# Kernel tuning notes

Hardware: AMD Instinct MI355X
Metric: run time of the kernel (lower is better)

The kernel has to match this reference:

```python
import jax, jax.numpy as jnp
import numpy as np

BQ, BK = 128, 64  # SpargeAttn-style Q/K block sizes
NEG = -1e30


def _block_mask(q, k, simthreshd1, cdfthreshd, scale):
    """Mean-similarity block selection: a (q-block, k-block) pair is pruned only
    when both blocks are self-similar (mean cosine sim to block mean exceeds the
    per-head simthreshd1) AND it is not in the top-CDF mass (cdfthreshd) of the
    compressed block-level softmax."""
    B, H, L, D = q.shape
    nq, nk = L // BQ, L // BK
    qb = q.reshape(B, H, nq, BQ, D)
    kb = k.reshape(B, H, nk, BK, D)
    qm = qb.mean(3)  # [B,H,nq,D] block means
    km = kb.mean(3)  # [B,H,nk,D]

    def blocksim(xb, xm):
        xn = xb / (jnp.linalg.norm(xb, axis=-1, keepdims=True) + 1e-6)
        mn = xm / (jnp.linalg.norm(xm, axis=-1, keepdims=True) + 1e-6)
        return jnp.einsum('bhntd,bhnd->bhnt', xn, mn).mean(-1)  # [B,H,n]

    th = simthreshd1[None, :, None]
    comp_q = blocksim(qb, qm) > th  # [B,H,nq] self-similar q blocks
    comp_k = blocksim(kb, km) > th  # [B,H,nk]

    # compressed attention over block means, then CDF-based top-mass selection
    p = jax.nn.softmax(jnp.einsum('bhqd,bhkd->bhqk', qm, km) * scale, axis=-1)
    order = jnp.argsort(-p, axis=-1)
    sp = jnp.take_along_axis(p, order, axis=-1)
    csum = jnp.cumsum(sp, axis=-1)
    keep_sorted = (csum - sp) < cdfthreshd[None, :, None, None]  # prefix covering tau
    rank = jnp.argsort(order, axis=-1)  # inverse permutation
    selected = jnp.take_along_axis(keep_sorted, rank, axis=-1)  # [B,H,nq,nk]

    return selected | ~(comp_q[..., :, None] & comp_k[..., None, :])


def setup_inputs() -> dict:
    key = jax.random.key(0)
    kq, kk, kv, kc = jax.random.split(key, 4)
    B, H, L, D = 1, 16, 2048, 64
    return {
        'q': jax.random.normal(kq, (B, H, L, D), dtype=jnp.float32),
        'k': jax.random.normal(kk, (B, H, L, D), dtype=jnp.float32),
        'v': jax.random.normal(kv, (B, H, L, D), dtype=jnp.float32),
        'simthreshd1': jnp.zeros((H,), dtype=jnp.float32),
        'cdfthreshd': jax.random.uniform(kc, (H,), dtype=jnp.float32),
    }


def reference(q, k, v, simthreshd1, cdfthreshd):
    B, H, L, D = q.shape
    scale = 1.0 / np.sqrt(D).astype(np.float32)
    # smooth_k: subtract per-(B,H) key mean (softmax-invariant shift, matches kernel)
    k = k - k.mean(axis=-2, keepdims=True)
    bmask = _block_mask(q, k, simthreshd1, cdfthreshd, scale)  # [B,H,nq,nk] bool
    mask_tok = jnp.repeat(jnp.repeat(bmask, BQ, axis=2), BK, axis=3)  # [B,H,L,L]
    s = jnp.einsum('bhqd,bhkd->bhqk', q, k) * scale
    s = jnp.where(mask_tok, s, NEG)
    p = jax.nn.softmax(s, axis=-1)
    return jnp.einsum('bhqk,bhkd->bhqd', p, v)
```

## Files before the change

kernel.cpp:

```cpp
#include <hip/hip_runtime.h>

#define HH 16
#define LL 2048
#define DD 64
#define BQ 128
#define BK 64
#define NQ (LL/BQ)
#define NK (LL/BK)
#define SCALE 0.125f
#define QSCALE (0.125f * 1.44269504f)

typedef __attribute__((ext_vector_type(8))) short s8v;
typedef __attribute__((ext_vector_type(4))) float f4v;

static __device__ __forceinline__ ushort f2bf(float x) {
    unsigned u = __float_as_uint(x);
    u += 0x7fff + ((u >> 16) & 1);
    return (ushort)(u >> 16);
}

#define GLOAD(src, dst) \
    __builtin_amdgcn_global_load_lds((const __attribute__((address_space(1))) unsigned int*)(src), \
                                     (__attribute__((address_space(3))) unsigned int*)(dst), 16, 0, 0)

__global__ void kmean1_kernel(const float* __restrict__ k, float* __restrict__ kpart) {
    int b = blockIdx.x;
    int h = blockIdx.y;
    int t = threadIdx.x;
    int d = t & 63, c = t >> 6;
    const float* kh = k + ((size_t)h*LL + (size_t)b*256) * DD;
    float s = 0.f;
    for (int l = c*64; l < c*64 + 64; ++l) s += kh[(size_t)l * DD + d];
    __shared__ float red[4][64];
    red[c][d] = s;
    __syncthreads();
    if (t < 64) kpart[((size_t)h*8 + b)*64 + t] = red[0][t]+red[1][t]+red[2][t]+red[3][t];
}

__global__ void qstat_kernel(const float* __restrict__ q, const float* __restrict__ simth,
                             float* __restrict__ qm, int* __restrict__ compq,
                             ushort* __restrict__ qb) {
    int qi = blockIdx.x, h = blockIdx.y;
    int t = threadIdx.x;
    size_t row = (size_t)h*LL + (size_t)qi*BQ + t;
    const float* rp = q + row * DD;
    float x[DD]; float n2 = 0.f;
    #pragma unroll
    for (int d = 0; d < DD; d += 4) {
        float4 v4 = *(const float4*)(rp + d);
        x[d]=v4.x; x[d+1]=v4.y; x[d+2]=v4.z; x[d+3]=v4.w;
        n2 += v4.x*v4.x + v4.y*v4.y + v4.z*v4.z + v4.w*v4.w;
    }
    #pragma unroll
    for (int d = 0; d < DD; d += 4) {
        ushort4 o;
        o.x = f2bf(x[d]*QSCALE);   o.y = f2bf(x[d+1]*QSCALE);
        o.z = f2bf(x[d+2]*QSCALE); o.w = f2bf(x[d+3]*QSCALE);
        *(ushort4*)(qb + row*DD + d) = o;
    }
    __shared__ float xs[BQ][DD+1];
    #pragma unroll
    for (int d = 0; d < DD; ++d) xs[t][d] = x[d];
    __syncthreads();
    __shared__ float mean[DD];
    if (t < DD) {
        float s = 0.f;
        for (int r = 0; r < BQ; ++r) s += xs[r][t];
        mean[t] = s * (1.0f/BQ);
    }
    __syncthreads();
    float dot = 0.f, m2 = 0.f;
    #pragma unroll
    for (int d = 0; d < DD; ++d) { dot += x[d]*mean[d]; m2 += mean[d]*mean[d]; }
    float cs = dot / ((sqrtf(n2) + 1e-6f) * (sqrtf(m2) + 1e-6f));
    __shared__ float red[BQ];
    red[t] = cs; __syncthreads();
    for (int sft = BQ/2; sft > 0; sft >>= 1) {
        if (t < sft) red[t] += red[t + sft];
        __syncthreads();
    }
    if (t == 0) compq[h*NQ + qi] = (red[0] * (1.0f/BQ)) > simth[h] ? 1 : 0;
    if (t < DD) qm[((size_t)h*NQ + qi)*DD + t] = mean[t];
}

__global__ void kstat_kernel(const float* __restrict__ k, const float* __restrict__ v,
                             const float* __restrict__ kpart, const float* __restrict__ simth,
                             float* __restrict__ km, int* __restrict__ compk,
                             ushort* __restrict__ kb, ushort* __restrict__ vTb) {
    int ki = blockIdx.x, h = blockIdx.y;
    int t = threadIdx.x;
    __shared__ float mu_s[DD];
    {
        float s = 0.f;
        #pragma unroll
        for (int b = 0; b < 8; ++b) s += kpart[((size_t)h*8 + b)*64 + t];
        mu_s[t] = s * (1.0f/LL);
    }
    __syncthreads();
    size_t row = (size_t)h*LL + (size_t)ki*BK + t;
    const float* rp = k + row * DD;
    float x[DD]; float n2 = 0.f;
    #pragma unroll
    for (int d = 0; d < DD; d += 4) {
        float4 v4 = *(const float4*)(rp + d);
        v4.x -= mu_s[d]; v4.y -= mu_s[d+1]; v4.z -= mu_s[d+2]; v4.w -= mu_s[d+3];
        x[d]=v4.x; x[d+1]=v4.y; x[d+2]=v4.z; x[d+3]=v4.w;
        n2 += v4.x*v4.x + v4.y*v4.y + v4.z*v4.z + v4.w*v4.w;
    }
    #pragma unroll
    for (int d = 0; d < DD; d += 4) {
        ushort4 o;
        o.x = f2bf(x[d]);   o.y = f2bf(x[d+1]);
        o.z = f2bf(x[d+2]); o.w = f2bf(x[d+3]);
        *(ushort4*)(kb + row*DD + d) = o;
    }
    __shared__ ushort vs[64][66];
    {
        const float* vp = v + row * DD;
        #pragma unroll
        for (int d = 0; d < DD; d += 4) {
            float4 v4 = *(const float4*)(vp + d);
            vs[t][d]   = f2bf(v4.x); vs[t][d+1] = f2bf(v4.y);
            vs[t][d+2] = f2bf(v4.z); vs[t][d+3] = f2bf(v4.w);
        }
    }
    __shared__ float xs[BK][DD+1];
    #pragma unroll
    for (int d = 0; d < DD; ++d) xs[t][d] = x[d];
    __syncthreads();
    {
        size_t vbase = ((size_t)h*DD + t)*LL + (size_t)ki*64;
        #pragma unroll
        for (int r8 = 0; r8 < 64; r8 += 8) {
            s8v o;
            #pragma unroll
            for (int e = 0; e < 8; ++e) o[e] = (short)vs[r8+e][t];
            *(s8v*)(vTb + vbase + r8) = o;
        }
    }
    __shared__ float mean[DD];
    {
        float s = 0.f;
        for (int r = 0; r < BK; ++r) s += xs[r][t];
        mean[t] = s * (1.0f/BK);
    }
    __syncthreads();
    float dot = 0.f, m2 = 0.f;
    #pragma unroll
    for (int d = 0; d < DD; ++d) { dot += x[d]*mean[d]; m2 += mean[d]*mean[d]; }
    float cs = dot / ((sqrtf(n2) + 1e-6f) * (sqrtf(m2) + 1e-6f));
    __shared__ float red[BK];
    red[t] = cs; __syncthreads();
    for (int sft = BK/2; sft > 0; sft >>= 1) {
        if (t < sft) red[t] += red[t + sft];
        __syncthreads();
    }
    if (t == 0) compk[h*NK + ki] = (red[0] * (1.0f/BK)) > simth[h] ? 1 : 0;
    km[((size_t)h*NK + ki)*DD + t] = mean[t];
}

__global__ void bmask_kernel(const float* __restrict__ qm, const float* __restrict__ km,
                             const int* __restrict__ compq, const int* __restrict__ compk,
                             const float* __restrict__ cdfth, unsigned* __restrict__ bmaskbits) {
    int qi = blockIdx.x, h = blockIdx.y;
    int j = threadIdx.x;
    __shared__ float ssh[NK];
    __shared__ float p[NK];
    const float* qv = qm + ((size_t)h*NQ + qi)*DD;
    const float* kv = km + ((size_t)h*NK + j)*DD;
    float s = 0.f;
    for (int d = 0; d < DD; ++d) s += qv[d]*kv[d];
    ssh[j] = s * SCALE;
    __syncthreads();
    float m = ssh[0];
    for (int i = 1; i < NK; ++i) m = fmaxf(m, ssh[i]);
    float den = 0.f;
    for (int i = 0; i < NK; ++i) den += expf(ssh[i] - m);
    p[j] = expf(ssh[j] - m) / den;
    __syncthreads();
    float pj = p[j];
    float mass = 0.f;
    for (int i = 0; i < NK; ++i) {
        float pi = p[i];
        if (pi > pj || (pi == pj && i < j)) mass += pi;
    }
    int sel = (mass < cdfth[h]) ? 1 : 0;
    int keep = (sel || !(compq[h*NQ+qi] && compk[h*NK+j])) ? 1 : 0;
    unsigned long long bal = __ballot(keep);
    if (j == 0) bmaskbits[h*NQ + qi] = (unsigned)bal;
}

__global__ __launch_bounds__(256, 2) void attn_kernel(
        const ushort* __restrict__ qb, const ushort* __restrict__ kb,
        const ushort* __restrict__ vTb, const unsigned* __restrict__ bmaskbits,
        float* __restrict__ out) {
    __shared__ __align__(16) ushort ldsK[2][64*64];
    __shared__ __align__(16) ushort ldsV[2][64*64];
    __shared__ __align__(16) ushort plds[4][16][72];

    int h    = blockIdx.y;
    int qi   = blockIdx.x >> 1;
    int half = blockIdx.x & 1;
    int tid  = threadIdx.x;
    int w    = tid >> 6;
    int l    = tid & 63;
    int lo = l & 15, hi = l >> 4;
    int r0 = qi*BQ + half*64 + w*16;

    unsigned msk = bmaskbits[h*NQ + qi];

    const ushort* qh = qb  + (size_t)h*LL*DD;
    const char*   kh = (const char*)(kb  + (size_t)h*LL*DD);
    const char*   vh = (const char*)(vTb + (size_t)h*DD*LL);

    int srow = l >> 3;
    int sgx  = ((l & 7) ^ srow) * 16;
    int c0 = 2*w, c1 = 2*w + 1;
    size_t ks0 = (size_t)(c0*8 + srow)*128 + sgx;
    size_t ks1 = (size_t)(c1*8 + srow)*128 + sgx;
    size_t vs0 = (size_t)(c0*8 + srow)*(LL*2) + sgx;
    size_t vs1 = (size_t)(c1*8 + srow)*(LL*2) + sgx;
    int dst0 = c0*1024, dst1 = c1*1024;

    int p0 = (hi)     ^ (lo & 7);
    int p1 = (4 + hi) ^ (lo & 7);
    int kidx0 = lo*64 + p0*8;
    int kidx1 = lo*64 + p1*8;

    s8v qa[2];
    #pragma unroll
    for (int kk = 0; kk < 2; ++kk)
        qa[kk] = *(const s8v*)(qh + (size_t)(r0 + lo)*DD + kk*32 + hi*8);

    f4v O[4];
    float mrun = -1e30f, lrun = 0.f;
    #pragma unroll
    for (int nd = 0; nd < 4; ++nd) O[nd] = (f4v){0.f, 0.f, 0.f, 0.f};

    auto stage = [&](int buf, int j) {
        const char* kj = kh + (size_t)j*8192;
        const char* vj = vh + (size_t)j*128;
        char* kd = (char*)&ldsK[buf][0];
        char* vd = (char*)&ldsV[buf][0];
        GLOAD(kj + ks0, kd + dst0);
        GLOAD(kj + ks1, kd + dst1);
        GLOAD(vj + vs0, vd + dst0);
        GLOAD(vj + vs1, vd + dst1);
    };

    auto compute = [&](const ushort* Kb, const ushort* Vb) {
        f4v S[4];
        #pragma unroll
        for (int ni = 0; ni < 4; ++ni) S[ni] = (f4v){0.f, 0.f, 0.f, 0.f};
        __builtin_amdgcn_s_setprio(1);
        #pragma unroll
        for (int ni = 0; ni < 4; ++ni) {
            s8v kf0 = *(const s8v*)(Kb + ni*1024 + kidx0);
            s8v kf1 = *(const s8v*)(Kb + ni*1024 + kidx1);
            S[ni] = __builtin_amdgcn_mfma_f32_16x16x32_bf16(kf0, qa[0], S[ni], 0, 0, 0);
            S[ni] = __builtin_amdgcn_mfma_f32_16x16x32_bf16(kf1, qa[1], S[ni], 0, 0, 0);
        }
        __builtin_amdgcn_s_setprio(0);
        float pm;
        {
            float a0 = fmaxf(fmaxf(S[0][0],S[0][1]), fmaxf(S[0][2],S[0][3]));
            float a1 = fmaxf(fmaxf(S[1][0],S[1][1]), fmaxf(S[1][2],S[1][3]));
            float a2 = fmaxf(fmaxf(S[2][0],S[2][1]), fmaxf(S[2][2],S[2][3]));
            float a3 = fmaxf(fmaxf(S[3][0],S[3][1]), fmaxf(S[3][2],S[3][3]));
            pm = fmaxf(fmaxf(a0,a1), fmaxf(a2,a3));
        }
        pm = fmaxf(pm, __shfl_xor(pm, 16));
        pm = fmaxf(pm, __shfl_xor(pm, 32));
        if (__any(pm > mrun + 8.0f)) {
            float mnew = fmaxf(mrun, pm);
            float alpha = __builtin_amdgcn_exp2f(mrun - mnew);
            lrun *= alpha;
            #pragma unroll
            for (int r = 0; r < 4; ++r) {
                float a = __shfl(alpha, hi*4 + r);
                #pragma unroll
                for (int nd = 0; nd < 4; ++nd) O[nd][r] *= a;
            }
            mrun = mnew;
        }
        f4v P4[4];
        float ps = 0.f;
        #pragma unroll
        for (int ni = 0; ni < 4; ++ni)
            #pragma unroll
            for (int r = 0; r < 4; ++r) {
                float p = __builtin_amdgcn_exp2f(S[ni][r] - mrun);
                P4[ni][r] = p;
                ps += p;
            }
        lrun += ps;
        #pragma unroll
        for (int ni = 0; ni < 4; ++ni) {
            unsigned c01, c23;
            asm("v_cvt_pk_bf16_f32 %0, %1, %2" : "=v"(c01) : "v"(P4[ni][0]), "v"(P4[ni][1]));
            asm("v_cvt_pk_bf16_f32 %0, %1, %2" : "=v"(c23) : "v"(P4[ni][2]), "v"(P4[ni][3]));
            *(uint2*)&plds[w][lo][ni*16 + hi*4] = make_uint2(c01, c23);
        }
        __builtin_amdgcn_s_setprio(1);
        #pragma unroll
        for (int kk = 0; kk < 2; ++kk) {
            s8v pa = *(const s8v*)&plds[w][lo][kk*32 + hi*8];
            int kidx = kk ? kidx1 : kidx0;
            #pragma unroll
            for (int nd = 0; nd < 4; ++nd) {
                s8v vf = *(const s8v*)(Vb + nd*1024 + kidx);
                O[nd] = __builtin_amdgcn_mfma_f32_16x16x32_bf16(pa, vf, O[nd], 0, 0, 0);
            }
        }
        __builtin_amdgcn_s_setprio(0);
    };

    int j0 = __ffs(msk) - 1; msk &= msk - 1;
    stage(0, j0);
    for (;;) {
        __syncthreads();
        int jn = msk ? __ffs(msk) - 1 : -1; msk &= msk - 1;
        if (jn >= 0) stage(1, jn);
        compute(&ldsK[0][0], &ldsV[0][0]);
        if (jn < 0) break;
        __syncthreads();
        int jm = msk ? __ffs(msk) - 1 : -1; msk &= msk - 1;
        if (jm >= 0) stage(0, jm);
        compute(&ldsK[1][0], &ldsV[1][0]);
        if (jm < 0) break;
    }

    float ltot = lrun;
    ltot += __shfl_xor(ltot, 16);
    ltot += __shfl_xor(ltot, 32);
    #pragma unroll
    for (int r = 0; r < 4; ++r) {
        float lr = __shfl(ltot, hi*4 + r);
        float inv = 1.0f / lr;
        int row = r0 + hi*4 + r;
        float* orow = out + ((size_t)h*LL + row)*DD;
        #pragma unroll
        for (int nd = 0; nd < 4; ++nd)
            orow[nd*16 + lo] = O[nd][r] * inv;
    }
}

extern "C" void kernel_launch(void* const* d_in, const int* in_sizes, int n_in,
                              void* d_out, int out_size, void* d_ws, size_t ws_size,
                              hipStream_t stream) {
    const float* q     = (const float*)d_in[0];
    const float* k     = (const float*)d_in[1];
    const float* v     = (const float*)d_in[2];
    const float* simth = (const float*)d_in[3];
    const float* cdfth = (const float*)d_in[4];
    float* out = (float*)d_out;

    float* ws    = (float*)d_ws;
    float* kpart = ws;
    float* qm    = kpart + HH*8*64;
    float* km    = qm + HH*NQ*DD;
    int*   compq = (int*)(km + HH*NK*DD);
    int*   compk = compq + HH*NQ;
    unsigned* bmb = (unsigned*)(compk + HH*NK);
    size_t off = (size_t)((char*)(bmb + HH*NQ) - (char*)d_ws);
    off = (off + 15) & ~(size_t)15;
    ushort* qbuf = (ushort*)((char*)d_ws + off);
    ushort* kbuf = qbuf + (size_t)HH*LL*DD;
    ushort* vTb  = kbuf + (size_t)HH*LL*DD;

    kmean1_kernel<<<dim3(8, HH), 256, 0, stream>>>(k, kpart);
    qstat_kernel<<<dim3(NQ, HH), BQ, 0, stream>>>(q, simth, qm, compq, qbuf);
    kstat_kernel<<<dim3(NK, HH), BK, 0, stream>>>(k, v, kpart, simth, km, compk, kbuf, vTb);
    bmask_kernel<<<dim3(NQ, HH), NK, 0, stream>>>(qm, km, compq, compk, cdfth, bmb);
    attn_kernel<<<dim3(NQ*2, HH), 256, 0, stream>>>(qbuf, kbuf, vTb, bmb, out);
}
```

Measured before the change: 81.81 us.

## Merge stat kernels, fold block-mask into attention, triple-buffer K/V loads

Merges the separate q and k statistics kernels into one launch, and the k path now uses 128 threads so V conversion runs alongside K processing. The block-mask computation moves into the attention kernel's prologue using wavefront shuffles, which removes the bmask launch and its global round-trip. The attention main loop goes from double to triple buffering, with explicit vmcnt waits and raw barriers, to keep more K/V loads in flight. The cost is extra LDS per block, which may reduce occupancy, and some redundant mask computation in each of the two attention blocks per q-tile.

```diff
diff --git a/kernel.cpp b/kernel.cpp
--- a/kernel.cpp
+++ b/kernel.cpp
@@ -22,6 +22,10 @@
 #define GLOAD(src, dst) \
     __builtin_amdgcn_global_load_lds((const __attribute__((address_space(1))) unsigned int*)(src), \
                                      (__attribute__((address_space(3))) unsigned int*)(dst), 16, 0, 0)
+
+#define VMWAIT4 do { asm volatile("s_waitcnt vmcnt(4)" ::: "memory"); __builtin_amdgcn_sched_barrier(0); } while(0)
+#define VMWAIT0 do { asm volatile("s_waitcnt vmcnt(0)" ::: "memory"); __builtin_amdgcn_sched_barrier(0); } while(0)
+#define BARRIER do { __builtin_amdgcn_s_barrier(); __builtin_amdgcn_sched_barrier(0); } while(0)
 
 __global__ void kmean1_kernel(const float* __restrict__ k, float* __restrict__ kpart) {
     int b = blockIdx.x;
@@ -37,166 +41,142 @@
     if (t < 64) kpart[((size_t)h*8 + b)*64 + t] = red[0][t]+red[1][t]+red[2][t]+red[3][t];
 }
 
-__global__ void qstat_kernel(const float* __restrict__ q, const float* __restrict__ simth,
-                             float* __restrict__ qm, int* __restrict__ compq,
-                             ushort* __restrict__ qb) {
-    int qi = blockIdx.x, h = blockIdx.y;
-    int t = threadIdx.x;
-    size_t row = (size_t)h*LL + (size_t)qi*BQ + t;
-    const float* rp = q + row * DD;
-    float x[DD]; float n2 = 0.f;
-    #pragma unroll
-    for (int d = 0; d < DD; d += 4) {
-        float4 v4 = *(const float4*)(rp + d);
-        x[d]=v4.x; x[d+1]=v4.y; x[d+2]=v4.z; x[d+3]=v4.w;
-        n2 += v4.x*v4.x + v4.y*v4.y + v4.z*v4.z + v4.w*v4.w;
+__global__ __launch_bounds__(128) void stats_kernel(
+        const float* __restrict__ q, const float* __restrict__ k, const float* __restrict__ v,
+        const float* __restrict__ kpart, const float* __restrict__ simth,
+        float* __restrict__ qm, float* __restrict__ km,
+        int* __restrict__ compq, int* __restrict__ compk,
+        ushort* __restrict__ qb, ushort* __restrict__ kb, ushort* __restrict__ vTb) {
+    __shared__ __align__(16) char smem[34304];
+    int h = blockIdx.y, t = threadIdx.x;
+
+    if ((int)blockIdx.x < NQ) {
+        int qi = blockIdx.x;
+        float (*xs)[DD+1] = (float(*)[DD+1])smem;
+        float* mean = (float*)(smem + 33280);
+        float* red  = (float*)(smem + 33536);
+        size_t row = (size_t)h*LL + (size_t)qi*BQ + t;
+        const float* rp = q + row * DD;
+        float x[DD]; float n2 = 0.f;
+        #pragma unroll
+        for (int d = 0; d < DD; d += 4) {
+            float4 v4 = *(const float4*)(rp + d);
+            x[d]=v4.x; x[d+1]=v4.y; x[d+2]=v4.z; x[d+3]=v4.w;
+            n2 += v4.x*v4.x + v4.y*v4.y + v4.z*v4.z + v4.w*v4.w;
+        }
+        #pragma unroll
+        for (int d = 0; d < DD; d += 4) {
+            ushort4 o;
+            o.x = f2bf(x[d]*QSCALE);   o.y = f2bf(x[d+1]*QSCALE);
+            o.z = f2bf(x[d+2]*QSCALE); o.w = f2bf(x[d+3]*QSCALE);
+            *(ushort4*)(qb + row*DD + d) = o;
+        }
+        #pragma unroll
+        for (int d = 0; d < DD; ++d) xs[t][d] = x[d];
+        __syncthreads();
+        if (t < DD) {
+            float s = 0.f;
+            for (int r = 0; r < BQ; ++r) s += xs[r][t];
+            mean[t] = s * (1.0f/BQ);
+        }
+        __syncthreads();
+        float dot = 0.f, m2 = 0.f;
+        #pragma unroll
+        for (int d = 0; d < DD; ++d) { dot += x[d]*mean[d]; m2 += mean[d]*mean[d]; }
+        float cs = dot / ((sqrtf(n2) + 1e-6f) * (sqrtf(m2) + 1e-6f));
+        red[t] = cs; __syncthreads();
+        for (int sft = BQ/2; sft > 0; sft >>= 1) {
+            if (t < sft) red[t] += red[t + sft];
+            __syncthreads();
+        }
+        if (t == 0) compq[h*NQ + qi] = (red[0] * (1.0f/BQ)) > simth[h] ? 1 : 0;
+        if (t < DD) qm[((size_t)h*NQ + qi)*DD + t] = mean[t];
+    } else {
+        int ki = blockIdx.x - NQ;
+        float* mu_s = (float*)smem;
+        float (*xs)[DD+1] = (float(*)[DD+1])(smem + 256);
+        ushort (*vs)[66]  = (ushort(*)[66])(smem + 256 + 16640);
+        float* mean = (float*)(smem + 256 + 16640 + 8448);
+        float* red  = (float*)(smem + 256 + 16640 + 8448 + 256);
+        if (t < 64) {
+            float s = 0.f;
+            #pragma unroll
+            for (int b = 0; b < 8; ++b) s += kpart[((size_t)h*8 + b)*64 + t];
+            mu_s[t] = s * (1.0f/LL);
+        }
+        __syncthreads();
+        size_t rowb = (size_t)h*LL + (size_t)ki*BK;
+        float x[DD]; float n2 = 0.f;
+        if (t < 64) {
+            const float* rp = k + (rowb + t) * DD;
+            #pragma unroll
+            for (int d = 0; d < DD; d += 4) {
+                float4 v4 = *(const float4*)(rp + d);
+                v4.x -= mu_s[d]; v4.y -= mu_s[d+1]; v4.z -= mu_s[d+2]; v4.w -= mu_s[d+3];
+                x[d]=v4.x; x[d+1]=v4.y; x[d+2]=v4.z; x[d+3]=v4.w;
+                n2 += v4.x*v4.x + v4.y*v4.y + v4.z*v4.z + v4.w*v4.w;
+            }
+            #pragma unroll
+            for (int d = 0; d < DD; d += 4) {
+                ushort4 o;
+                o.x = f2bf(x[d]);   o.y = f2bf(x[d+1]);
+                o.z = f2bf(x[d+2]); o.w = f2bf(x[d+3]);
+                *(ushort4*)(kb + (rowb + t)*DD + d) = o;
+            }
+            #pragma unroll
+            for (int d = 0; d < DD; ++d) xs[t][d] = x[d];
+        } else {
+            int tk = t - 64;
+            const float* vp = v + (rowb + tk) * DD;
+            #pragma unroll
+            for (int d = 0; d < DD; d += 4) {
+                float4 v4 = *(const float4*)(vp + d);
+                vs[tk][d]   = f2bf(v4.x); vs[tk][d+1] = f2bf(v4.y);
+                vs[tk][d+2] = f2bf(v4.z); vs[tk][d+3] = f2bf(v4.w);
+            }
+        }
+        __syncthreads();
+        if (t < 64) {
+            size_t vbase = ((size_t)h*DD + t)*LL + (size_t)ki*64;
+            #pragma unroll
+            for (int r8 = 0; r8 < 64; r8 += 8) {
+                s8v o;
+                #pragma unroll
+                for (int e = 0; e < 8; ++e) o[e] = (short)vs[r8+e][t];
+                *(s8v*)(vTb + vbase + r8) = o;
+            }
+            float s = 0.f;
+            for (int r = 0; r < BK; ++r) s += xs[r][t];
+            mean[t] = s * (1.0f/BK);
+        }
+        __syncthreads();
+        if (t < 64) {
+            float dot = 0.f, m2 = 0.f;
+            #pragma unroll
+            for (int d = 0; d < DD; ++d) { dot += x[d]*mean[d]; m2 += mean[d]*mean[d]; }
+            float cs = dot / ((sqrtf(n2) + 1e-6f) * (sqrtf(m2) + 1e-6f));
+            red[t] = cs;
+        }
+        __syncthreads();
+        for (int sft = 32; sft > 0; sft >>= 1) {
+            if (t < sft) red[t] += red[t + sft];
+            __syncthreads();
+        }
+        if (t == 0) compk[h*NK + ki] = (red[0] * (1.0f/BK)) > simth[h] ? 1 : 0;
+        if (t < 64) km[((size_t)h*NK + ki)*DD + t] = mean[t];
     }
-    #pragma unroll
-    for (int d = 0; d < DD; d += 4) {
-        ushort4 o;
-        o.x = f2bf(x[d]*QSCALE);   o.y = f2bf(x[d+1]*QSCALE);
-        o.z = f2bf(x[d+2]*QSCALE); o.w = f2bf(x[d+3]*QSCALE);
-        *(ushort4*)(qb + row*DD + d) = o;
-    }
-    __shared__ float xs[BQ][DD+1];
-    #pragma unroll
-    for (int d = 0; d < DD; ++d) xs[t][d] = x[d];
-    __syncthreads();
-    __shared__ float mean[DD];
-    if (t < DD) {
-        float s = 0.f;
-        for (int r = 0; r < BQ; ++r) s += xs[r][t];
-        mean[t] = s * (1.0f/BQ);
-    }
-    __syncthreads();
-    float dot = 0.f, m2 = 0.f;
-    #pragma unroll
-    for (int d = 0; d < DD; ++d) { dot += x[d]*mean[d]; m2 += mean[d]*mean[d]; }
-    float cs = dot / ((sqrtf(n2) + 1e-6f) * (sqrtf(m2) + 1e-6f));
-    __shared__ float red[BQ];
-    red[t] = cs; __syncthreads();
-    for (int sft = BQ/2; sft > 0; sft >>= 1) {
-        if (t < sft) red[t] += red[t + sft];
-        __syncthreads();
-    }
-    if (t == 0) compq[h*NQ + qi] = (red[0] * (1.0f/BQ)) > simth[h] ? 1 : 0;
-    if (t < DD) qm[((size_t)h*NQ + qi)*DD + t] = mean[t];
-}
-
-__global__ void kstat_kernel(const float* __restrict__ k, const float* __restrict__ v,
-                             const float* __restrict__ kpart, const float* __restrict__ simth,
-                             float* __restrict__ km, int* __restrict__ compk,
-                             ushort* __restrict__ kb, ushort* __restrict__ vTb) {
-    int ki = blockIdx.x, h = blockIdx.y;
-    int t = threadIdx.x;
-    __shared__ float mu_s[DD];
-    {
-        float s = 0.f;
-        #pragma unroll
-        for (int b = 0; b < 8; ++b) s += kpart[((size_t)h*8 + b)*64 + t];
-        mu_s[t] = s * (1.0f/LL);
-    }
-    __syncthreads();
-    size_t row = (size_t)h*LL + (size_t)ki*BK + t;
-    const float* rp = k + row * DD;
-    float x[DD]; float n2 = 0.f;
-    #pragma unroll
-    for (int d = 0; d < DD; d += 4) {
-        float4 v4 = *(const float4*)(rp + d);
-        v4.x -= mu_s[d]; v4.y -= mu_s[d+1]; v4.z -= mu_s[d+2]; v4.w -= mu_s[d+3];
-        x[d]=v4.x; x[d+1]=v4.y; x[d+2]=v4.z; x[d+3]=v4.w;
-        n2 += v4.x*v4.x + v4.y*v4.y + v4.z*v4.z + v4.w*v4.w;
-    }
-    #pragma unroll
-    for (int d = 0; d < DD; d += 4) {
-        ushort4 o;
-        o.x = f2bf(x[d]);   o.y = f2bf(x[d+1]);
-        o.z = f2bf(x[d+2]); o.w = f2bf(x[d+3]);
-        *(ushort4*)(kb + row*DD + d) = o;
-    }
-    __shared__ ushort vs[64][66];
-    {
-        const float* vp = v + row * DD;
-        #pragma unroll
-        for (int d = 0; d < DD; d += 4) {
-            float4 v4 = *(const float4*)(vp + d);
-            vs[t][d]   = f2bf(v4.x); vs[t][d+1] = f2bf(v4.y);
-            vs[t][d+2] = f2bf(v4.z); vs[t][d+3] = f2bf(v4.w);
-        }
-    }
-    __shared__ float xs[BK][DD+1];
-    #pragma unroll
-    for (int d = 0; d < DD; ++d) xs[t][d] = x[d];
-    __syncthreads();
-    {
-        size_t vbase = ((size_t)h*DD + t)*LL + (size_t)ki*64;
-        #pragma unroll
-        for (int r8 = 0; r8 < 64; r8 += 8) {
-            s8v o;
-            #pragma unroll
-            for (int e = 0; e < 8; ++e) o[e] = (short)vs[r8+e][t];
-            *(s8v*)(vTb + vbase + r8) = o;
-        }
-    }
-    __shared__ float mean[DD];
-    {
-        float s = 0.f;
-        for (int r = 0; r < BK; ++r) s += xs[r][t];
-        mean[t] = s * (1.0f/BK);
-    }
-    __syncthreads();
-    float dot = 0.f, m2 = 0.f;
-    #pragma unroll
-    for (int d = 0; d < DD; ++d) { dot += x[d]*mean[d]; m2 += mean[d]*mean[d]; }
-    float cs = dot / ((sqrtf(n2) + 1e-6f) * (sqrtf(m2) + 1e-6f));
-    __shared__ float red[BK];
-    red[t] = cs; __syncthreads();
-    for (int sft = BK/2; sft > 0; sft >>= 1) {
-        if (t < sft) red[t] += red[t + sft];
-        __syncthreads();
-    }
-    if (t == 0) compk[h*NK + ki] = (red[0] * (1.0f/BK)) > simth[h] ? 1 : 0;
-    km[((size_t)h*NK + ki)*DD + t] = mean[t];
-}
-
-__global__ void bmask_kernel(const float* __restrict__ qm, const float* __restrict__ km,
-                             const int* __restrict__ compq, const int* __restrict__ compk,
-                             const float* __restrict__ cdfth, unsigned* __restrict__ bmaskbits) {
-    int qi = blockIdx.x, h = blockIdx.y;
-    int j = threadIdx.x;
-    __shared__ float ssh[NK];
-    __shared__ float p[NK];
-    const float* qv = qm + ((size_t)h*NQ + qi)*DD;
-    const float* kv = km + ((size_t)h*NK + j)*DD;
-    float s = 0.f;
-    for (int d = 0; d < DD; ++d) s += qv[d]*kv[d];
-    ssh[j] = s * SCALE;
-    __syncthreads();
-    float m = ssh[0];
-    for (int i = 1; i < NK; ++i) m = fmaxf(m, ssh[i]);
-    float den = 0.f;
-    for (int i = 0; i < NK; ++i) den += expf(ssh[i] - m);
-    p[j] = expf(ssh[j] - m) / den;
-    __syncthreads();
-    float pj = p[j];
-    float mass = 0.f;
-    for (int i = 0; i < NK; ++i) {
-        float pi = p[i];
-        if (pi > pj || (pi == pj && i < j)) mass += pi;
-    }
-    int sel = (mass < cdfth[h]) ? 1 : 0;
-    int keep = (sel || !(compq[h*NQ+qi] && compk[h*NK+j])) ? 1 : 0;
-    unsigned long long bal = __ballot(keep);
-    if (j == 0) bmaskbits[h*NQ + qi] = (unsigned)bal;
 }
 
 __global__ __launch_bounds__(256, 2) void attn_kernel(
         const ushort* __restrict__ qb, const ushort* __restrict__ kb,
-        const ushort* __restrict__ vTb, const unsigned* __restrict__ bmaskbits,
-        float* __restrict__ out) {
-    __shared__ __align__(16) ushort ldsK[2][64*64];
-    __shared__ __align__(16) ushort ldsV[2][64*64];
+        const ushort* __restrict__ vTb,
+        const float* __restrict__ qm, const float* __restrict__ km,
+        const int* __restrict__ compq, const int* __restrict__ compk,
+        const float* __restrict__ cdfth, float* __restrict__ out) {
+    __shared__ __align__(16) ushort ldsK[3][64*64];
+    __shared__ __align__(16) ushort ldsV[3][64*64];
     __shared__ __align__(16) ushort plds[4][16][72];
+    __shared__ unsigned mskS;
 
     int h    = blockIdx.y;
     int qi   = blockIdx.x >> 1;
@@ -207,11 +187,40 @@
     int lo = l & 15, hi = l >> 4;
     int r0 = qi*BQ + half*64 + w*16;
 
-    unsigned msk = bmaskbits[h*NQ + qi];
-
     const ushort* qh = qb  + (size_t)h*LL*DD;
     const char*   kh = (const char*)(kb  + (size_t)h*LL*DD);
     const char*   vh = (const char*)(vTb + (size_t)h*DD*LL);
+
+    s8v qa[2];
+    #pragma unroll
+    for (int kk = 0; kk < 2; ++kk)
+        qa[kk] = *(const s8v*)(qh + (size_t)(r0 + lo)*DD + kk*32 + hi*8);
+
+    if (tid < 64) {
+        int j = l & 31;
+        const float* qv = qm + ((size_t)h*NQ + qi)*DD;
+        const float* kv = km + ((size_t)h*NK + j)*DD;
+        float s = 0.f;
+        for (int d = 0; d < DD; ++d) s += qv[d]*kv[d];
+        s *= SCALE;
+        float m = s;
+        #pragma unroll
+        for (int xm = 1; xm <= 16; xm <<= 1) m = fmaxf(m, __shfl_xor(m, xm, 32));
+        float e = expf(s - m);
+        float den = 0.f;
+        for (int i = 0; i < 32; ++i) den += __shfl(e, i, 32);
+        float p = e / den;
+        float mass = 0.f;
+        for (int i = 0; i < 32; ++i) {
+            float pi = __shfl(p, i, 32);
+            if (pi > p || (pi == p && i < j)) mass += pi;
+        }
+        int keep = (mass < cdfth[h]) || !(compq[h*NQ+qi] && compk[h*NK+j]);
+        unsigned long long bal = __ballot(keep != 0);
+        if (l == 0) mskS = (unsigned)bal;
+    }
+    __syncthreads();
+    unsigned msk = mskS;
 
     int srow = l >> 3;
     int sgx  = ((l & 7) ^ srow) * 16;
@@ -226,11 +235,6 @@
     int p1 = (4 + hi) ^ (lo & 7);
     int kidx0 = lo*64 + p0*8;
     int kidx1 = lo*64 + p1*8;
-
-    s8v qa[2];
-    #pragma unroll
-    for (int kk = 0; kk < 2; ++kk)
-        qa[kk] = *(const s8v*)(qh + (size_t)(r0 + lo)*DD + kk*32 + hi*8);
 
     f4v O[4];
     float mrun = -1e30f, lrun = 0.f;
@@ -315,19 +319,30 @@
         __builtin_amdgcn_s_setprio(0);
     };
 
-    int j0 = __ffs(msk) - 1; msk &= msk - 1;
-    stage(0, j0);
+    int ja = __ffs(msk) - 1; msk &= msk - 1;
+    stage(0, ja);
+    int jb = msk ? __ffs(msk) - 1 : -1; msk &= msk - 1;
+    if (jb >= 0) stage(1, jb);
+    int jc;
     for (;;) {
-        __syncthreads();
-        int jn = msk ? __ffs(msk) - 1 : -1; msk &= msk - 1;
-        if (jn >= 0) stage(1, jn);
+        if (jb >= 0) { VMWAIT4; } else { VMWAIT0; }
+        BARRIER;
+        jc = msk ? __ffs(msk) - 1 : -1; msk &= msk - 1;
+        if (jc >= 0) stage(2, jc);
         compute(&ldsK[0][0], &ldsV[0][0]);
-        if (jn < 0) break;
-        __syncthreads();
-        int jm = msk ? __ffs(msk) - 1 : -1; msk &= msk - 1;
-        if (jm >= 0) stage(0, jm);
+        if (jb < 0) break;
+        if (jc >= 0) { VMWAIT4; } else { VMWAIT0; }
+        BARRIER;
+        ja = msk ? __ffs(msk) - 1 : -1; msk &= msk - 1;
+        if (ja >= 0) stage(0, ja);
         compute(&ldsK[1][0], &ldsV[1][0]);
-        if (jm < 0) break;
+        if (jc < 0) break;
+        if (ja >= 0) { VMWAIT4; } else { VMWAIT0; }
+        BARRIER;
+        jb = msk ? __ffs(msk) - 1 : -1; msk &= msk - 1;
+        if (jb >= 0) stage(1, jb);
+        compute(&ldsK[2][0], &ldsV[2][0]);
+        if (ja < 0) break;
     }
 
     float ltot = lrun;
@@ -361,16 +376,16 @@
     float* km    = qm + HH*NQ*DD;
     int*   compq = (int*)(km + HH*NK*DD);
     int*   compk = compq + HH*NQ;
-    unsigned* bmb = (unsigned*)(compk + HH*NK);
-    size_t off = (size_t)((char*)(bmb + HH*NQ) - (char*)d_ws);
+    size_t off = (size_t)((char*)(compk + HH*NK) - (char*)d_ws);
     off = (off + 15) & ~(size_t)15;
     ushort* qbuf = (ushort*)((char*)d_ws + off);
     ushort* kbuf = qbuf + (size_t)HH*LL*DD;
     ushort* vTb  = kbuf + (size_t)HH*LL*DD;
 
     kmean1_kernel<<<dim3(8, HH), 256, 0, stream>>>(k, kpart);
-    qstat_kernel<<<dim3(NQ, HH), BQ, 0, stream>>>(q, simth, qm, compq, qbuf);
-    kstat_kernel<<<dim3(NK, HH), BK, 0, stream>>>(k, v, kpart, simth, km, compk, kbuf, vTb);
-    bmask_kernel<<<dim3(NQ, HH), NK, 0, stream>>>(qm, km, compq, compk, cdfth, bmb);
-    attn_kernel<<<dim3(NQ*2, HH), 256, 0, stream>>>(qbuf, kbuf, vTb, bmb, out);
-}
+    stats_kernel<<<dim3(NQ + NK, HH), 128, 0, stream>>>(q, k, v, kpart, simth,
+                                                        qm, km, compq, compk,
+                                                        qbuf, kbuf, vTb);
+    attn_kernel<<<dim3(NQ*2, HH), 256, 0, stream>>>(qbuf, kbuf, vTb,
+                                                    qm, km, compq, compk, cdfth, out);
+}
```

New measurement: 78.23 us. 1.05x faster.
